# Performance work log

Measured on AMD Instinct MI355X. Metric: run time of the kernel, lower is better.

Reference implementation:

```python
import jax, jax.numpy as jnp
import numpy as np

B = 262144
HID = 256
HEADS = 8


def setup_inputs() -> dict:
    key = jax.random.key(0)
    ks = jax.random.split(key, 8)
    s = 1.0 / np.sqrt(HID)
    return {
        "fine_messages": jax.random.normal(ks[0], (B, HID), jnp.float32),
        "coarse_messages": jax.random.normal(ks[1], (B, HID), jnp.float32),
        "motif_features": jax.random.normal(ks[2], (B, HID), jnp.float32),
        "Wq": jax.random.normal(ks[3], (HID, HID), jnp.float32) * s,
        "Wk": jax.random.normal(ks[4], (HID, HID), jnp.float32) * s,
        "Wv": jax.random.normal(ks[5], (HID, HID), jnp.float32) * s,
        "Wo": jax.random.normal(ks[6], (HID, HID), jnp.float32) * s,
        "bo": jax.random.normal(ks[7], (HID,), jnp.float32) * s,
        "heads": HEADS,
    }


def reference(fine_messages, coarse_messages, motif_features, Wq, Wk, Wv, Wo, bo, heads):
    b, hid = motif_features.shape
    d_k = hid // heads
    # K/V share the same pre-projection input: [fine; coarse] -> (B, 2, hid)
    kv_in = jnp.stack([fine_messages, coarse_messages], axis=1)
    # torch Linear(x) = x @ W.T (no bias on q/k/v projections)
    q = (motif_features @ Wq.T).reshape(b, heads, d_k)          # (B, H, d_k) single query
    k = (kv_in @ Wk.T).reshape(b, 2, heads, d_k)                # (B, 2, H, d_k)
    v = (kv_in @ Wv.T).reshape(b, 2, heads, d_k)
    # NOTE: original divides by d_k, not sqrt(d_k)
    scores = jnp.einsum("bhd,bshd->bhs", q, k) / d_k            # (B, H, 2)
    att = jax.nn.softmax(scores, axis=-1)
    out = jnp.einsum("bhs,bshd->bhd", att, v).reshape(b, hid)   # (B, hid)
    return out @ Wo.T + bo
```

## Files before the change

### kernel.cpp

```cpp
#include <hip/hip_runtime.h>

#define B_TOT 262144
#define HID   256
#define NHEAD 8
#define BR    64
#define NTHR  256

typedef __bf16 bf16_t;
typedef __attribute__((ext_vector_type(8))) __bf16 bf16x8;
typedef __attribute__((ext_vector_type(4))) __bf16 bf16x4;
typedef __attribute__((ext_vector_type(4))) float  f32x4;

#define QKV_BYTES (384 * 1024)

#define PHASE_SYNC(N)                                                  \
  do {                                                                 \
    asm volatile("s_waitcnt vmcnt(" #N ") lgkmcnt(0)" ::: "memory");   \
    __builtin_amdgcn_s_barrier();                                      \
    __builtin_amdgcn_sched_barrier(0);                                 \
  } while (0)

static __device__ __forceinline__ f32x4 mfma16(bf16x8 a, bf16x8 b, f32x4 c) {
  return __builtin_amdgcn_mfma_f32_16x16x32_bf16(a, b, c, 0, 0, 0);
}

static __device__ __forceinline__ bf16x8 cvt8(float4 a, float4 b) {
  bf16x8 r;
  r[0] = (bf16_t)a.x; r[1] = (bf16_t)a.y; r[2] = (bf16_t)a.z; r[3] = (bf16_t)a.w;
  r[4] = (bf16_t)b.x; r[5] = (bf16_t)b.y; r[6] = (bf16_t)b.z; r[7] = (bf16_t)b.w;
  return r;
}

static __device__ __forceinline__ bf16x8 pin8(bf16x8 v) {
  f32x4 t = __builtin_bit_cast(f32x4, v);
  asm volatile("" : "+v"(t));
  return __builtin_bit_cast(bf16x8, t);
}

typedef __attribute__((address_space(3))) void lds_void;
typedef __attribute__((address_space(1))) void gbl_void;
static __device__ __forceinline__ void gload_lds16(const void* g, void* l) {
  __builtin_amdgcn_global_load_lds((gbl_void*)g, (lds_void*)l, 16, 0, 0);
}

__global__ __launch_bounds__(256) void pack_weights(
    const float* __restrict__ Wq, const float* __restrict__ Wk,
    const float* __restrict__ Wv, const float* __restrict__ Wo,
    bf16_t* __restrict__ ws) {
  const int t     = blockIdx.x * 256 + threadIdx.x;
  const int lane  = t & 63;
  const int chunk = t >> 6;
  const int l15 = lane & 15, lg = lane >> 4;
  const float* src;
  int row, col;
  if (chunk < 384) {
    const int slot = chunk % 6;
    const int hk   = chunk / 6;
    const int wi = slot >> 1, half = slot & 1;
    const int h = hk >> 3, ks = hk & 7;
    src = (wi == 0) ? Wq : (wi == 1) ? Wk : Wv;
    row = h * 32 + (l15 >> 2) * 8 + half * 4 + (l15 & 3);
    col = ks * 32 + lg * 8;
  } else {
    const int c  = chunk - 384;
    const int ks = c >> 4, jt = c & 15;
    src = Wo;
    row = jt * 16 + l15;
    col = ks * 32 + lg * 8;
  }
  const float* p = src + (size_t)row * HID + col;
  const float4 a = *(const float4*)p;
  const float4 b = *(const float4*)(p + 4);
  *(bf16x8*)(ws + (size_t)t * 8) = cvt8(a, b);
}

__global__ __launch_bounds__(NTHR, 2) void fused_local_aug(
    const float* __restrict__ fine, const float* __restrict__ coarse,
    const float* __restrict__ motif, const bf16_t* __restrict__ wpk,
    const float* __restrict__ bo, float* __restrict__ out) {
  __shared__ char wbuf[73728];

  const int tid  = threadIdx.x;
  const int lane = tid & 63;
  const int wave = tid >> 6;
  const int l15  = lane & 15;
  const int lg   = lane >> 4;
  const size_t row0 = (size_t)blockIdx.x * BR;
  const size_t mrow = row0 + wave * 16 + l15;

  auto stage = [&](int ph) {
    char* dst = wbuf + (ph % 3) * 24576 + tid * 16;
    if (ph < 16) {
      const char* src = (const char*)wpk + (ph >> 1) * 49152 + (ph & 1) * 24576 + tid * 16;
#pragma unroll
      for (int i = 0; i < 6; ++i)
        gload_lds16(src + i * 4096, dst + i * 4096);
    } else {
      const char* src = (const char*)wpk + QKV_BYTES + (ph - 16) * 16384 + tid * 16;
#pragma unroll
      for (int i = 0; i < 4; ++i)
        gload_lds16(src + i * 4096, dst + i * 4096);
    }
  };

  stage(0);
  stage(1);

  bf16x8 xm[8], xf[8], xc[8];
  {
    const float* pm = motif  + mrow * HID + lg * 8;
    const float* pf = fine   + mrow * HID + lg * 8;
    const float* pc = coarse + mrow * HID + lg * 8;
#pragma unroll
    for (int s = 0; s < 8; ++s) {
      xm[s] = pin8(cvt8(*(const float4*)(pm + s * 32), *(const float4*)(pm + s * 32 + 4)));
      xf[s] = pin8(cvt8(*(const float4*)(pf + s * 32), *(const float4*)(pf + s * 32 + 4)));
      xc[s] = pin8(cvt8(*(const float4*)(pc + s * 32), *(const float4*)(pc + s * 32 + 4)));
    }
  }
  __syncthreads();

  bf16x4 mo0[NHEAD], mo1[NHEAD];

#pragma unroll
  for (int h = 0; h < NHEAD; ++h) {
    f32x4 aQ0{}, aQ1{}, aK10{}, aK11{}, aK20{}, aK21{}, aV10{}, aV11{}, aV20{}, aV21{};
#pragma unroll
    for (int half = 0; half < 2; ++half) {
      const int p = 2 * h + half;
      if (p > 0) {
        if (p == 15) { PHASE_SYNC(4); }
        else         { PHASE_SYNC(6); }
      }
      stage(p + 2);
      const char* pb = wbuf + (p % 3) * 24576 + lane * 16;
#pragma unroll
      for (int kk = 0; kk < 4; ++kk) {
        const int ks = half * 4 + kk;
        const char* q = pb + kk * 6144;
        bf16x8 q0 = *(const bf16x8*)(q);
        bf16x8 q1 = *(const bf16x8*)(q + 1024);
        bf16x8 k0 = *(const bf16x8*)(q + 2048);
        bf16x8 k1 = *(const bf16x8*)(q + 3072);
        bf16x8 v0 = *(const bf16x8*)(q + 4096);
        bf16x8 v1 = *(const bf16x8*)(q + 5120);
        aQ0  = mfma16(q0, xm[ks], aQ0);   aQ1  = mfma16(q1, xm[ks], aQ1);
        aK10 = mfma16(k0, xf[ks], aK10);  aK11 = mfma16(k1, xf[ks], aK11);
        aK20 = mfma16(k0, xc[ks], aK20);  aK21 = mfma16(k1, xc[ks], aK21);
        aV10 = mfma16(v0, xf[ks], aV10);  aV11 = mfma16(v1, xf[ks], aV11);
        aV20 = mfma16(v0, xc[ks], aV20);  aV21 = mfma16(v1, xc[ks], aV21);
      }
    }
    float s1 = 0.f, s2 = 0.f;
#pragma unroll
    for (int r = 0; r < 4; ++r) {
      s1 += aQ0[r] * aK10[r] + aQ1[r] * aK11[r];
      s2 += aQ0[r] * aK20[r] + aQ1[r] * aK21[r];
    }
    s1 += __shfl_xor(s1, 16); s1 += __shfl_xor(s1, 32);
    s2 += __shfl_xor(s2, 16); s2 += __shfl_xor(s2, 32);
    s1 *= (1.0f / 32.0f);  s2 *= (1.0f / 32.0f);
    const float mx = fmaxf(s1, s2);
    const float e1 = __expf(s1 - mx), e2 = __expf(s2 - mx);
    const float a1 = e1 / (e1 + e2);
    const float a2 = 1.0f - a1;
#pragma unroll
    for (int r = 0; r < 4; ++r) {
      mo0[h][r] = (bf16_t)(a1 * aV10[r] + a2 * aV20[r]);
      mo1[h][r] = (bf16_t)(a1 * aV11[r] + a2 * aV21[r]);
    }
  }

  bf16x8 mfrag[NHEAD];
#pragma unroll
  for (int h = 0; h < NHEAD; ++h) {
    bf16x8 t;
    t[0] = mo0[h][0]; t[1] = mo0[h][1]; t[2] = mo0[h][2]; t[3] = mo0[h][3];
    t[4] = mo1[h][0]; t[5] = mo1[h][1]; t[6] = mo1[h][2]; t[7] = mo1[h][3];
    mfrag[h] = t;
  }

  f32x4 acc[16];
#pragma unroll
  for (int jt = 0; jt < 16; ++jt) acc[jt] = f32x4{0.f, 0.f, 0.f, 0.f};

#pragma unroll
  for (int wp = 0; wp < 8; ++wp) {
    const int p = 16 + wp;
    if (wp == 7) { PHASE_SYNC(0); }
    else         { PHASE_SYNC(4); }
    if (wp < 6) stage(p + 2);
    bf16x8 mf = mfrag[wp];
    const char* pb = wbuf + (p % 3) * 24576 + lane * 16;
#pragma unroll
    for (int jt = 0; jt < 16; ++jt) {
      bf16x8 wf = *(const bf16x8*)(pb + jt * 1024);
      acc[jt] = mfma16(wf, mf, acc[jt]);
    }
  }

#pragma unroll
  for (int jt = 0; jt < 16; ++jt) {
    const int jj = jt * 16 + lg * 4;
    const float4 b4 = *(const float4*)(bo + jj);
    f32x4 o;
    o[0] = acc[jt][0] + b4.x;
    o[1] = acc[jt][1] + b4.y;
    o[2] = acc[jt][2] + b4.z;
    o[3] = acc[jt][3] + b4.w;
    __builtin_nontemporal_store(o, (f32x4*)(out + mrow * HID + jj));
  }
}

extern "C" void kernel_launch(void* const* d_in, const int* in_sizes, int n_in,
                              void* d_out, int out_size, void* d_ws, size_t ws_size,
                              hipStream_t stream) {
  (void)in_sizes; (void)n_in; (void)ws_size; (void)out_size;
  const float* fine   = (const float*)d_in[0];
  const float* coarse = (const float*)d_in[1];
  const float* motif  = (const float*)d_in[2];
  const float* Wq     = (const float*)d_in[3];
  const float* Wk     = (const float*)d_in[4];
  const float* Wv     = (const float*)d_in[5];
  const float* Wo     = (const float*)d_in[6];
  const float* bo     = (const float*)d_in[7];
  float* out          = (float*)d_out;
  bf16_t* wpk         = (bf16_t*)d_ws;

  pack_weights<<<128, 256, 0, stream>>>(Wq, Wk, Wv, Wo, wpk);
  fused_local_aug<<<B_TOT / BR, NTHR, 0, stream>>>(fine, coarse, motif, wpk, bo, out);
}
```

Measured before the change: 357.1 us.

## Split QKV staging into uniform 16KB phases to cut LDS and raise occupancy

Repacks the Q/K/V weights so each head is staged as three separate 16KB phases (Q, K, V) instead of two 24KB mixed phases. This shrinks the triple-buffered LDS from 72KB to 48KB and raises the launch-bounds occupancy target from 2 to 3 blocks per CU, with the aim of hiding memory latency better. It also wraps the MFMA loops in s_setprio and builds the bf16 fragments in place. The trade-offs are more barriers per head and tighter register limits, which could cause spills.

```diff
diff --git a/kernel.cpp b/kernel.cpp
--- a/kernel.cpp
+++ b/kernel.cpp
@@ -11,7 +11,6 @@
 typedef __attribute__((ext_vector_type(4))) __bf16 bf16x4;
 typedef __attribute__((ext_vector_type(4))) float  f32x4;
 
-#define QKV_BYTES (384 * 1024)
 
 #define PHASE_SYNC(N)                                                  \
   do {                                                                 \
@@ -54,11 +53,11 @@
   const float* src;
   int row, col;
   if (chunk < 384) {
-    const int slot = chunk % 6;
-    const int hk   = chunk / 6;
-    const int wi = slot >> 1, half = slot & 1;
-    const int h = hk >> 3, ks = hk & 7;
-    src = (wi == 0) ? Wq : (wi == 1) ? Wk : Wv;
+    const int ph = chunk >> 4;
+    const int c  = chunk & 15;
+    const int h = ph / 3, w = ph % 3;
+    const int ks = c >> 1, half = c & 1;
+    src = (w == 0) ? Wq : (w == 1) ? Wk : Wv;
     row = h * 32 + (l15 >> 2) * 8 + half * 4 + (l15 & 3);
     col = ks * 32 + lg * 8;
   } else {
@@ -74,11 +73,11 @@
   *(bf16x8*)(ws + (size_t)t * 8) = cvt8(a, b);
 }
 
-__global__ __launch_bounds__(NTHR, 2) void fused_local_aug(
+__global__ __launch_bounds__(NTHR, 3) void fused_local_aug(
     const float* __restrict__ fine, const float* __restrict__ coarse,
     const float* __restrict__ motif, const bf16_t* __restrict__ wpk,
     const float* __restrict__ bo, float* __restrict__ out) {
-  __shared__ char wbuf[73728];
+  __shared__ char wbuf[49152];
 
   const int tid  = threadIdx.x;
   const int lane = tid & 63;
@@ -89,18 +88,11 @@
   const size_t mrow = row0 + wave * 16 + l15;
 
   auto stage = [&](int ph) {
-    char* dst = wbuf + (ph % 3) * 24576 + tid * 16;
-    if (ph < 16) {
-      const char* src = (const char*)wpk + (ph >> 1) * 49152 + (ph & 1) * 24576 + tid * 16;
-#pragma unroll
-      for (int i = 0; i < 6; ++i)
-        gload_lds16(src + i * 4096, dst + i * 4096);
-    } else {
-      const char* src = (const char*)wpk + QKV_BYTES + (ph - 16) * 16384 + tid * 16;
-#pragma unroll
-      for (int i = 0; i < 4; ++i)
-        gload_lds16(src + i * 4096, dst + i * 4096);
-    }
+    char* dst = wbuf + (ph % 3) * 16384 + tid * 16;
+    const char* src = (const char*)wpk + (size_t)ph * 16384 + tid * 16;
+#pragma unroll
+    for (int i = 0; i < 4; ++i)
+      gload_lds16(src + i * 4096, dst + i * 4096);
   };
 
   stage(0);
@@ -120,36 +112,60 @@
   }
   __syncthreads();
 
-  bf16x4 mo0[NHEAD], mo1[NHEAD];
+  bf16x8 mfrag[NHEAD];
 
 #pragma unroll
   for (int h = 0; h < NHEAD; ++h) {
     f32x4 aQ0{}, aQ1{}, aK10{}, aK11{}, aK20{}, aK21{}, aV10{}, aV11{}, aV20{}, aV21{};
-#pragma unroll
-    for (int half = 0; half < 2; ++half) {
-      const int p = 2 * h + half;
-      if (p > 0) {
-        if (p == 15) { PHASE_SYNC(4); }
-        else         { PHASE_SYNC(6); }
+
+    {
+      const int p = 3 * h;
+      if (p > 0) PHASE_SYNC(4);
+      stage(p + 2);
+      const char* pb = wbuf + (p % 3) * 16384 + lane * 16;
+      __builtin_amdgcn_s_setprio(1);
+#pragma unroll
+      for (int ks = 0; ks < 8; ++ks) {
+        bf16x8 q0 = *(const bf16x8*)(pb + ks * 2048);
+        bf16x8 q1 = *(const bf16x8*)(pb + ks * 2048 + 1024);
+        aQ0 = mfma16(q0, xm[ks], aQ0);
+        aQ1 = mfma16(q1, xm[ks], aQ1);
       }
+      __builtin_amdgcn_s_setprio(0);
+    }
+    {
+      const int p = 3 * h + 1;
+      PHASE_SYNC(4);
       stage(p + 2);
-      const char* pb = wbuf + (p % 3) * 24576 + lane * 16;
-#pragma unroll
-      for (int kk = 0; kk < 4; ++kk) {
-        const int ks = half * 4 + kk;
-        const char* q = pb + kk * 6144;
-        bf16x8 q0 = *(const bf16x8*)(q);
-        bf16x8 q1 = *(const bf16x8*)(q + 1024);
-        bf16x8 k0 = *(const bf16x8*)(q + 2048);
-        bf16x8 k1 = *(const bf16x8*)(q + 3072);
-        bf16x8 v0 = *(const bf16x8*)(q + 4096);
-        bf16x8 v1 = *(const bf16x8*)(q + 5120);
-        aQ0  = mfma16(q0, xm[ks], aQ0);   aQ1  = mfma16(q1, xm[ks], aQ1);
-        aK10 = mfma16(k0, xf[ks], aK10);  aK11 = mfma16(k1, xf[ks], aK11);
-        aK20 = mfma16(k0, xc[ks], aK20);  aK21 = mfma16(k1, xc[ks], aK21);
-        aV10 = mfma16(v0, xf[ks], aV10);  aV11 = mfma16(v1, xf[ks], aV11);
-        aV20 = mfma16(v0, xc[ks], aV20);  aV21 = mfma16(v1, xc[ks], aV21);
+      const char* pb = wbuf + (p % 3) * 16384 + lane * 16;
+      __builtin_amdgcn_s_setprio(1);
+#pragma unroll
+      for (int ks = 0; ks < 8; ++ks) {
+        bf16x8 k0 = *(const bf16x8*)(pb + ks * 2048);
+        bf16x8 k1 = *(const bf16x8*)(pb + ks * 2048 + 1024);
+        aK10 = mfma16(k0, xf[ks], aK10);
+        aK11 = mfma16(k1, xf[ks], aK11);
+        aK20 = mfma16(k0, xc[ks], aK20);
+        aK21 = mfma16(k1, xc[ks], aK21);
       }
+      __builtin_amdgcn_s_setprio(0);
+    }
+    {
+      const int p = 3 * h + 2;
+      PHASE_SYNC(4);
+      stage(p + 2);
+      const char* pb = wbuf + (p % 3) * 16384 + lane * 16;
+      __builtin_amdgcn_s_setprio(1);
+#pragma unroll
+      for (int ks = 0; ks < 8; ++ks) {
+        bf16x8 v0 = *(const bf16x8*)(pb + ks * 2048);
+        bf16x8 v1 = *(const bf16x8*)(pb + ks * 2048 + 1024);
+        aV10 = mfma16(v0, xf[ks], aV10);
+        aV11 = mfma16(v1, xf[ks], aV11);
+        aV20 = mfma16(v0, xc[ks], aV20);
+        aV21 = mfma16(v1, xc[ks], aV21);
+      }
+      __builtin_amdgcn_s_setprio(0);
     }
     float s1 = 0.f, s2 = 0.f;
 #pragma unroll
@@ -164,19 +180,12 @@
     const float e1 = __expf(s1 - mx), e2 = __expf(s2 - mx);
     const float a1 = e1 / (e1 + e2);
     const float a2 = 1.0f - a1;
+    bf16x8 t;
 #pragma unroll
     for (int r = 0; r < 4; ++r) {
-      mo0[h][r] = (bf16_t)(a1 * aV10[r] + a2 * aV20[r]);
-      mo1[h][r] = (bf16_t)(a1 * aV11[r] + a2 * aV21[r]);
-    }
-  }
-
-  bf16x8 mfrag[NHEAD];
-#pragma unroll
-  for (int h = 0; h < NHEAD; ++h) {
-    bf16x8 t;
-    t[0] = mo0[h][0]; t[1] = mo0[h][1]; t[2] = mo0[h][2]; t[3] = mo0[h][3];
-    t[4] = mo1[h][0]; t[5] = mo1[h][1]; t[6] = mo1[h][2]; t[7] = mo1[h][3];
+      t[r]     = (bf16_t)(a1 * aV10[r] + a2 * aV20[r]);
+      t[r + 4] = (bf16_t)(a1 * aV11[r] + a2 * aV21[r]);
+    }
     mfrag[h] = t;
   }
 
@@ -186,17 +195,19 @@
 
 #pragma unroll
   for (int wp = 0; wp < 8; ++wp) {
-    const int p = 16 + wp;
+    const int p = 24 + wp;
     if (wp == 7) { PHASE_SYNC(0); }
     else         { PHASE_SYNC(4); }
     if (wp < 6) stage(p + 2);
     bf16x8 mf = mfrag[wp];
-    const char* pb = wbuf + (p % 3) * 24576 + lane * 16;
+    const char* pb = wbuf + (p % 3) * 16384 + lane * 16;
+    __builtin_amdgcn_s_setprio(1);
 #pragma unroll
     for (int jt = 0; jt < 16; ++jt) {
       bf16x8 wf = *(const bf16x8*)(pb + jt * 1024);
       acc[jt] = mfma16(wf, mf, acc[jt]);
     }
+    __builtin_amdgcn_s_setprio(0);
   }
 
 #pragma unroll
```

Measured after the change: 522.3 us. +46.3%, slower.
